# Optimization experiments

Measured on AMD Instinct MI355X. Metric: run time of the kernel, lower is better.

## Reference

```python
import jax, jax.numpy as jnp
import numpy as np

B_, H_, W_, DMODEL = 4, 56, 56, 96
DSTATE = 16
DIN = int(2.0 * DMODEL)      # d_inner = ssm_ratio * d_model
RANK = int(np.ceil(DMODEL / 16))  # dt_rank 'auto'
K = 4                         # 4 scan directions


def setup_inputs() -> dict:
    key = jax.random.key(0)
    ks = jax.random.split(key, 8)
    f = lambda k, shape, s=0.02: jax.random.normal(k, shape, jnp.float32) * s
    x = jax.random.normal(ks[0], (B_, H_, W_, DMODEL), jnp.float32)
    in_proj_w = f(ks[1], (2 * DIN, DMODEL))
    conv_w = f(ks[2], (DIN, 1, 3, 3), 0.1)          # depthwise 3x3
    conv_b = jnp.zeros((DIN,), jnp.float32)
    x_proj_weight = f(ks[3], (K, RANK + 2 * DSTATE, DIN))
    dt_projs_weight = f(ks[4], (K, DIN, RANK), 0.1)
    # dt bias = inverse-softplus of dt sampled log-uniform in [1e-3, 0.1]
    dt = jnp.exp(jax.random.uniform(ks[5], (K, DIN)) * (np.log(0.1) - np.log(0.001)) + np.log(0.001))
    dt_projs_bias = dt + jnp.log(-jnp.expm1(-dt))
    A_logs = jnp.log(jnp.tile(jnp.arange(1, DSTATE + 1, dtype=jnp.float32)[None, :], (K * DIN, 1)))
    Ds = jnp.ones((K * DIN,), jnp.float32)
    ln_gamma = jnp.ones((DIN,), jnp.float32)
    ln_beta = jnp.zeros((DIN,), jnp.float32)
    out_proj_w = f(ks[6], (DMODEL, DIN))
    return dict(x=x, in_proj_w=in_proj_w, conv_w=conv_w, conv_b=conv_b,
                x_proj_weight=x_proj_weight, dt_projs_weight=dt_projs_weight,
                dt_projs_bias=dt_projs_bias, A_logs=A_logs, Ds=Ds,
                ln_gamma=ln_gamma, ln_beta=ln_beta, out_proj_w=out_proj_w)


def _ss2d(x, in_proj_w, conv_w, conv_b, x_proj_weight, dt_projs_weight,
          dt_projs_bias, A_logs, Ds, ln_gamma, ln_beta, out_proj_w):
    B, H, W, _ = x.shape
    L, D, N = H * W, DIN, DSTATE
    # input projection, split into x and gate z
    xz = x @ in_proj_w.T                                   # [B,H,W,2D]
    xc, z = jnp.split(xz, 2, axis=-1)
    z = jax.nn.silu(z)
    # depthwise 3x3 conv (NCHW) + SiLU
    xc = xc.transpose(0, 3, 1, 2)                          # [B,D,H,W]
    xc = jax.lax.conv_general_dilated(
        xc, conv_w, (1, 1), 'SAME',
        dimension_numbers=('NCHW', 'OIHW', 'NCHW'),
        feature_group_count=D) + conv_b[None, :, None, None]
    xc = jax.nn.silu(xc)
    # 4-directional cross scan: HW, WH, and their reverses
    x_hw = xc.reshape(B, D, L)
    x_wh = xc.transpose(0, 1, 3, 2).reshape(B, D, L)
    x2 = jnp.stack([x_hw, x_wh], axis=1)                   # [B,2,D,L]
    xs = jnp.concatenate([x2, jnp.flip(x2, axis=-1)], axis=1)  # [B,K,D,L]
    # per-direction projections to (dt_rank, B, C)
    x_dbl = jnp.einsum('bkdl,kcd->bkcl', xs, x_proj_weight)
    dts, Bs, Cs = jnp.split(x_dbl, [RANK, RANK + N], axis=2)   # [B,K,R|N|N,L]
    dts = jnp.einsum('bkrl,kdr->bkdl', dts, dt_projs_weight)   # [B,K,D,L]
    A = -jnp.exp(A_logs).reshape(K, D, N)
    delta = jax.nn.softplus(dts + dt_projs_bias[None, :, :, None])  # [B,K,D,L]
    # selective state-space scan over L
    u_t = xs.transpose(3, 0, 1, 2)     # [L,B,K,D]
    d_t = delta.transpose(3, 0, 1, 2)  # [L,B,K,D]
    B_t = Bs.transpose(3, 0, 1, 2)     # [L,B,K,N]
    C_t = Cs.transpose(3, 0, 1, 2)     # [L,B,K,N]

    def step(h, inp):
        dt_, u_, b_, c_ = inp
        dA = jnp.exp(dt_[..., None] * A)                       # [B,K,D,N]
        h = dA * h + dt_[..., None] * b_[:, :, None, :] * u_[..., None]
        y = jnp.einsum('bkdn,bkn->bkd', h, c_)
        return h, y

    h0 = jnp.zeros((B, K, D, N), jnp.float32)
    _, ys = jax.lax.scan(step, h0, (d_t, u_t, B_t, C_t))       # ys: [L,B,K,D]
    out_y = ys.transpose(1, 2, 3, 0) + Ds.reshape(K, D)[None, :, :, None] * xs  # [B,K,D,L]
    # merge the 4 directions back into HW order
    inv_y = jnp.flip(out_y[:, 2:4], axis=-1)                   # [B,2,D,L]
    wh_y = out_y[:, 1].reshape(B, D, W, H).transpose(0, 1, 3, 2).reshape(B, D, L)
    invwh_y = inv_y[:, 1].reshape(B, D, W, H).transpose(0, 1, 3, 2).reshape(B, D, L)
    y = out_y[:, 0] + inv_y[:, 0] + wh_y + invwh_y             # [B,D,L]
    y = y.transpose(0, 2, 1)                                   # [B,L,D]
    mu = y.mean(-1, keepdims=True)
    var = y.var(-1, keepdims=True)
    y = (y - mu) * jax.lax.rsqrt(var + 1e-5) * ln_gamma + ln_beta
    y = y.reshape(B, H, W, D) * z
    return y @ out_proj_w.T                                    # [B,H,W,d_model]


def reference(x, in_proj_w, conv_w, conv_b, x_proj_weight, dt_projs_weight,
              dt_projs_bias, A_logs, Ds, ln_gamma, ln_beta, out_proj_w):
    return _ss2d(x, in_proj_w, conv_w, conv_b, x_proj_weight, dt_projs_weight,
                 dt_projs_bias, A_logs, Ds, ln_gamma, ln_beta, out_proj_w)
```

## Files before the change

### kernel.cpp

```cpp
#include <hip/hip_runtime.h>
#include <math.h>

typedef __attribute__((ext_vector_type(2))) float f32x2;
typedef unsigned short u16;

constexpr int BB  = 4;
constexpr int HH  = 56;
constexpr int WW  = 56;
constexpr int CM  = 96;
constexpr int DD  = 192;
constexpr int NS  = 16;
constexpr int KK  = 4;
constexpr int LL  = HH * WW;
constexpr int CH  = 16;
constexpr int NCH = LL / CH;
constexpr int GC  = 7;
constexpr int G   = NCH / GC;
constexpr int PCH = 64;
constexpr int PNCH = LL / PCH;
constexpr int XDS = 40;
constexpr int MR  = 32;
constexpr int YS  = 196;

static __device__ __forceinline__ float siluf(float x) {
  return x / (1.f + __expf(-x));
}
static __device__ __forceinline__ u16 f2bf(float x) {
  unsigned u = __float_as_uint(x);
  u += 0x7fffu + ((u >> 16) & 1u);
  return (u16)(u >> 16);
}
static __device__ __forceinline__ float bf2f(u16 h) {
  return __uint_as_float(((unsigned)h) << 16);
}
static __device__ __forceinline__ unsigned pack2bf(float a, float b) {
  return ((unsigned)f2bf(b) << 16) | f2bf(a);
}
static __device__ __forceinline__ f32x2 up2bf(unsigned v) {
  return (f32x2){__uint_as_float(v << 16),
                 __uint_as_float(v & 0xffff0000u)};
}

__global__ __launch_bounds__(256) void k_prep(
    const float* __restrict__ ipw, const float* __restrict__ xpw,
    float* __restrict__ wTi, float* __restrict__ wtp) {
  int idx = blockIdx.x * 256 + threadIdx.x;
  if (idx < 96 * 384) {
    int k96 = idx / 384, n = idx % 384;
    wTi[idx] = ipw[n * 96 + k96];
  }
  int j = idx - 96 * 384;
  if (j >= 0 && j < KK * DD * 40) {
    int k = j / (DD * 40);
    int r = j % (DD * 40);
    int d = r / 40, ci = r % 40;
    wtp[j] = (ci < 38) ? xpw[((size_t)k * 38 + ci) * DD + d] : 0.f;
  }
}

__global__ __launch_bounds__(256) void k_inproj(
    const float* __restrict__ x, const float* __restrict__ wTi,
    u16* __restrict__ xc16, u16* __restrict__ z16) {
  __shared__ float a[64 * 97];
  const int tid = threadIdx.x;
  const int m0 = blockIdx.x * 64;
  const int y  = blockIdx.y;
  const float4* xv = (const float4*)(x + (size_t)m0 * 96);
#pragma unroll
  for (int i = 0; i < 6; ++i) {
    int idx = tid + i * 256;
    int m = idx / 24, q = idx % 24;
    float4 v = xv[idx];
    a[m * 97 + 4 * q + 0] = v.x; a[m * 97 + 4 * q + 1] = v.y;
    a[m * 97 + 4 * q + 2] = v.z; a[m * 97 + 4 * q + 3] = v.w;
  }
  __syncthreads();
  const int lane = tid & 63;
  const int wid = __builtin_amdgcn_readfirstlane(threadIdx.x >> 6);
  const float* wrow0 = wTi + y * 96 + wid * 24;
  float acc[24];
#pragma unroll
  for (int j = 0; j < 24; ++j) acc[j] = 0.f;
  const float* arow = a + lane * 97;
#pragma unroll 4
  for (int k = 0; k < 96; ++k) {
    float u = arow[k];
    const float* wr = wrow0 + (size_t)k * 384;
#pragma unroll
    for (int j = 0; j < 24; ++j) acc[j] = fmaf(wr[j], u, acc[j]);
  }
  __syncthreads();
#pragma unroll
  for (int j = 0; j < 24; ++j) a[lane * 97 + wid * 24 + j] = acc[j];
  __syncthreads();
  const bool isz = (y >= 2);
  u16* dst = isz ? z16 : xc16;
  const int c0 = (y & 1) * 96;
#pragma unroll
  for (int i = 0; i < 6; ++i) {
    int idx = tid + i * 256;
    int m = idx / 24, q = idx % 24;
    float4 v;
    v.x = a[m * 97 + 4 * q + 0]; v.y = a[m * 97 + 4 * q + 1];
    v.z = a[m * 97 + 4 * q + 2]; v.w = a[m * 97 + 4 * q + 3];
    if (isz) { v.x = siluf(v.x); v.y = siluf(v.y);
               v.z = siluf(v.z); v.w = siluf(v.w); }
    *(uint2*)(dst + (size_t)(m0 + m) * DD + c0 + 4 * q) =
        make_uint2(pack2bf(v.x, v.y), pack2bf(v.z, v.w));
  }
}

__global__ __launch_bounds__(256) void k_conv(
    const u16* __restrict__ xc16, const float* __restrict__ cw,
    const float* __restrict__ cb, u16* __restrict__ xhw16) {
  const int idx = blockIdx.x * 256 + threadIdx.x;
  const int d = idx % DD;
  int t = idx / DD;
  const int w = t % WW;
  t /= WW;
  const int h = t % HH;
  const int b = t / HH;
  const u16* src = xc16 + (size_t)b * LL * DD;
  float acc = cb[d];
#pragma unroll
  for (int dh = -1; dh <= 1; ++dh) {
    int hh = h + dh;
    if (hh < 0 || hh >= HH) continue;
#pragma unroll
    for (int dw = -1; dw <= 1; ++dw) {
      int ww2 = w + dw;
      if (ww2 < 0 || ww2 >= WW) continue;
      acc = fmaf(cw[d * 9 + (dh + 1) * 3 + (dw + 1)],
                 bf2f(src[((size_t)hh * WW + ww2) * DD + d]), acc);
    }
  }
  xhw16[idx] = f2bf(siluf(acc));
}

__global__ __launch_bounds__(256) void k_xdbl(
    const u16* __restrict__ xhw16, const float* __restrict__ wtp,
    u16* __restrict__ xdbl16) {
  const int blk = blockIdx.x;
  const int b = blk / (KK * PNCH);
  const int k = (blk / PNCH) % KK;
  const int c = blk % PNCH;
  const int l0 = c * PCH;
  const bool rev = (k >= 2);
  const int pos = threadIdx.x & 63;
  const int cg = __builtin_amdgcn_readfirstlane(threadIdx.x >> 6);
  int tg = l0 + pos;
  int lg = rev ? (LL - 1 - tg) : tg;
  int row = (k & 1) ? ((lg % HH) * WW + lg / HH) : lg;
  const u16* ur = xhw16 + (size_t)b * LL * DD + (size_t)row * DD;
  const float* wbase = wtp + (size_t)k * DD * 40 + cg * 10;
  float acc[10];
#pragma unroll
  for (int q = 0; q < 10; ++q) acc[q] = 0.f;
#pragma unroll 2
  for (int d8 = 0; d8 < 24; ++d8) {
    uint4 uv = *(const uint4*)(ur + d8 * 8);
    f32x2 u01 = up2bf(uv.x), u23 = up2bf(uv.y);
    f32x2 u45 = up2bf(uv.z), u67 = up2bf(uv.w);
    const float* w0 = wbase + (size_t)(d8 * 8) * 40;
#pragma unroll
    for (int q = 0; q < 10; ++q) acc[q] = fmaf(w0[q],       u01.x, acc[q]);
#pragma unroll
    for (int q = 0; q < 10; ++q) acc[q] = fmaf(w0[40 + q],  u01.y, acc[q]);
#pragma unroll
    for (int q = 0; q < 10; ++q) acc[q] = fmaf(w0[80 + q],  u23.x, acc[q]);
#pragma unroll
    for (int q = 0; q < 10; ++q) acc[q] = fmaf(w0[120 + q], u23.y, acc[q]);
#pragma unroll
    for (int q = 0; q < 10; ++q) acc[q] = fmaf(w0[160 + q], u45.x, acc[q]);
#pragma unroll
    for (int q = 0; q < 10; ++q) acc[q] = fmaf(w0[200 + q], u45.y, acc[q]);
#pragma unroll
    for (int q = 0; q < 10; ++q) acc[q] = fmaf(w0[240 + q], u67.x, acc[q]);
#pragma unroll
    for (int q = 0; q < 10; ++q) acc[q] = fmaf(w0[280 + q], u67.y, acc[q]);
  }
  u16* dst = xdbl16 + ((size_t)(b * KK + k) * LL + l0 + pos) * XDS;
#pragma unroll
  for (int q = 0; q < 10; ++q) {
    int ci = cg * 10 + q;
    int col = ci + (ci >= 6 ? 2 : 0);
    dst[col] = f2bf(acc[q]);
  }
}

static __device__ __forceinline__ int row_init(int k, bool rev, int l0,
                                               int& hh, int& ww) {
  int tg = rev ? (LL - 1 - l0) : l0;
  if (k & 1) {
    hh = tg % HH;
    ww = tg / HH;
    return hh * WW + ww;
  }
  return tg;
}
static __device__ __forceinline__ int row_next(int k, bool rev, int row,
                                               int& hh, int& ww) {
  if (k & 1) {
    if (!rev) { if (++hh == HH) { hh = 0; ++ww; } }
    else      { if (--hh < 0) { hh = HH - 1; --ww; } }
    return hh * WW + ww;
  }
  return rev ? row - 1 : row + 1;
}

__global__ __launch_bounds__(192) void k_scan1(
    const u16* __restrict__ xhw16, const u16* __restrict__ xdbl16,
    const float* __restrict__ dtw, const float* __restrict__ dtb,
    float* __restrict__ Qc, u16* __restrict__ Sc16) {
  __shared__ float us[CH * DD];
  const int blk = blockIdx.x;
  const int b = blk / (KK * NCH);
  const int k = (blk / NCH) % KK;
  const int c = blk % NCH;
  const int l0 = c * CH;
  const bool rev = (k >= 2);
  const int d = threadIdx.x;
  const int bk = b * KK + k;
  {
    const u16* uplane = xhw16 + (size_t)b * LL * DD;
    float tmp[CH];
    int hh, ww;
    int row = row_init(k, rev, l0, hh, ww);
#pragma unroll
    for (int t = 0; t < CH; ++t) {
      tmp[t] = bf2f(uplane[(size_t)row * DD + d]);
      row = row_next(k, rev, row, hh, ww);
    }
#pragma unroll
    for (int t = 0; t < CH; ++t) us[t * DD + d] = tmp[t];
  }
  float w2[6];
#pragma unroll
  for (int r = 0; r < 6; ++r) w2[r] = dtw[((size_t)k * DD + d) * 6 + r];
  const float bias = dtb[k * DD + d];
  f32x2 h2[8];
#pragma unroll
  for (int m = 0; m < 8; ++m) h2[m] = (f32x2){0.f, 0.f};
  float sumd = 0.f;
  const u16* xrow = xdbl16 + ((size_t)bk * LL + l0) * XDS;
  __syncthreads();
#pragma unroll
  for (int t = 0; t < CH; ++t, xrow += XDS) {
    uint4 uv0 = *(const uint4*)(xrow);
    uint4 uv1 = *(const uint4*)(xrow + 8);
    uint4 uv2 = *(const uint4*)(xrow + 16);
    f32x2 d01 = up2bf(uv0.x), d23 = up2bf(uv0.y), d45 = up2bf(uv0.z);
    float u = us[t * DD + d];
    float draw = bias;
    draw = fmaf(w2[0], d01.x, draw);
    draw = fmaf(w2[1], d01.y, draw);
    draw = fmaf(w2[2], d23.x, draw);
    draw = fmaf(w2[3], d23.y, draw);
    draw = fmaf(w2[4], d45.x, draw);
    draw = fmaf(w2[5], d45.y, draw);
    float e = __expf(draw);
    float p = __builtin_amdgcn_rcpf(1.f + e);
    float delta = (draw < 15.f) ? -__logf(p) : draw;
    sumd += delta;
    float du = delta * u;
    f32x2 duv = {du, du};
    float ps = p * p;
    f32x2 pw = {p, ps};
    f32x2 q2 = {ps, ps};
    f32x2 bp[8] = {up2bf(uv1.x), up2bf(uv1.y), up2bf(uv1.z), up2bf(uv1.w),
                   up2bf(uv2.x), up2bf(uv2.y), up2bf(uv2.z), up2bf(uv2.w)};
#pragma unroll
    for (int m = 0; m < 8; ++m) {
      h2[m] = pw * h2[m] + duv * bp[m];
      pw = pw * q2;
    }
  }
  size_t qi = ((size_t)bk * NCH + c) * DD + d;
  Qc[qi] = sumd;
  unsigned* sp = (unsigned*)(Sc16 + qi * 16);
#pragma unroll
  for (int m = 0; m < 8; ++m) sp[m] = pack2bf(h2[m].x, h2[m].y);
}

__global__ __launch_bounds__(256) void k_pfxA(
    const float* __restrict__ Qc, const u16* __restrict__ Sc16,
    u16* __restrict__ Ag16, u16* __restrict__ Sg16) {
  int flat = blockIdx.x * 256 + threadIdx.x;
  int n = flat & 15;
  int d = (flat >> 4) % DD;
  int g = (flat / (NS * DD)) % G;
  int bk = flat / (NS * DD * G);
  const float en = -(float)(n + 1);
  size_t cbase = (size_t)bk * NCH + (size_t)g * GC;
  float q[GC], s[GC];
#pragma unroll
  for (int i = 0; i < GC; ++i) {
    size_t ci = (cbase + i) * DD + d;
    q[i] = Qc[ci];
    s[i] = bf2f(Sc16[ci * 16 + n]);
  }
  float qsum = 0.f, S = 0.f;
#pragma unroll
  for (int i = 0; i < GC; ++i) {
    qsum += q[i];
    S = fmaf(__expf(en * q[i]), S, s[i]);
  }
  Ag16[flat] = f2bf(__expf(en * qsum));
  Sg16[flat] = f2bf(S);
}

__global__ __launch_bounds__(256) void k_pfxB(
    const u16* __restrict__ Ag16, const u16* __restrict__ Sg16,
    u16* __restrict__ Hg16) {
  int flat = blockIdx.x * 256 + threadIdx.x;
  int dn = flat % (DD * NS);
  int bk = flat / (DD * NS);
  const size_t base0 = (size_t)bk * G * DD * NS + dn;
  const size_t gs = DD * NS;
  float av[G], sv[G];
#pragma unroll
  for (int g2 = 0; g2 < G; ++g2) {
    av[g2] = bf2f(Ag16[base0 + (size_t)g2 * gs]);
    sv[g2] = bf2f(Sg16[base0 + (size_t)g2 * gs]);
  }
  float h = 0.f;
#pragma unroll
  for (int g2 = 0; g2 < G; ++g2) {
    Hg16[base0 + (size_t)g2 * gs] = f2bf(h);
    h = fmaf(av[g2], h, sv[g2]);
  }
}

__global__ __launch_bounds__(192) void k_scan2(
    const u16* __restrict__ xhw16, const u16* __restrict__ xdbl16,
    const u16* __restrict__ Hg16, const float* __restrict__ Qc,
    const u16* __restrict__ Sc16, const float* __restrict__ dtw,
    const float* __restrict__ dtb, const float* __restrict__ Ds,
    u16* __restrict__ y16) {
  __shared__ float us[CH * DD];
  const int blk = blockIdx.x;
  const int b = blk / (KK * NCH);
  const int k = (blk / NCH) % KK;
  const int c = blk % NCH;
  const int g = c / GC;
  const int l0 = c * CH;
  const bool rev = (k >= 2);
  const int d = threadIdx.x;
  const int bk = b * KK + k;
  {
    const u16* uplane = xhw16 + (size_t)b * LL * DD;
    float tmp[CH];
    int hh, ww;
    int row = row_init(k, rev, l0, hh, ww);
#pragma unroll
    for (int t = 0; t < CH; ++t) {
      tmp[t] = bf2f(uplane[(size_t)row * DD + d]);
      row = row_next(k, rev, row, hh, ww);
    }
#pragma unroll
    for (int t = 0; t < CH; ++t) us[t * DD + d] = tmp[t];
  }
  float w2[6];
#pragma unroll
  for (int r = 0; r < 6; ++r) w2[r] = dtw[((size_t)k * DD + d) * 6 + r];
  const float bias = dtb[k * DD + d];
  const float dsd = Ds[k * DD + d];
  f32x2 h2[8];
  {
    const u16* hp = Hg16 + (((size_t)bk * G + g) * DD + d) * NS;
    uint4 a0 = *(const uint4*)hp;
    uint4 a1 = *(const uint4*)(hp + 8);
    h2[0] = up2bf(a0.x); h2[1] = up2bf(a0.y);
    h2[2] = up2bf(a0.z); h2[3] = up2bf(a0.w);
    h2[4] = up2bf(a1.x); h2[5] = up2bf(a1.y);
    h2[6] = up2bf(a1.z); h2[7] = up2bf(a1.w);
  }
  for (int i = g * GC; i < c; ++i) {
    size_t ci = ((size_t)bk * NCH + i) * DD + d;
    float r = __expf(-Qc[ci]);
    const u16* sp = Sc16 + ci * 16;
    uint4 s0 = *(const uint4*)sp;
    uint4 s1 = *(const uint4*)(sp + 8);
    f32x2 sv[8] = {up2bf(s0.x), up2bf(s0.y), up2bf(s0.z), up2bf(s0.w),
                   up2bf(s1.x), up2bf(s1.y), up2bf(s1.z), up2bf(s1.w)};
    float r2 = r * r;
    f32x2 pw = {r, r2};
    f32x2 q2 = {r2, r2};
#pragma unroll
    for (int m = 0; m < 8; ++m) {
      h2[m] = pw * h2[m] + sv[m];
      pw = pw * q2;
    }
  }
  u16* yplane = y16 + (size_t)bk * LL * DD + d;
  const u16* xrow = xdbl16 + ((size_t)bk * LL + l0) * XDS;
  int hh, ww;
  int row = row_init(k, rev, l0, hh, ww);
  __syncthreads();
#pragma unroll
  for (int t = 0; t < CH; ++t, xrow += XDS) {
    uint4 uv0 = *(const uint4*)(xrow);
    uint4 uv1 = *(const uint4*)(xrow + 8);
    uint4 uv2 = *(const uint4*)(xrow + 16);
    uint4 uv3 = *(const uint4*)(xrow + 24);
    uint4 uv4 = *(const uint4*)(xrow + 32);
    f32x2 d01 = up2bf(uv0.x), d23 = up2bf(uv0.y), d45 = up2bf(uv0.z);
    float u = us[t * DD + d];
    float draw = bias;
    draw = fmaf(w2[0], d01.x, draw);
    draw = fmaf(w2[1], d01.y, draw);
    draw = fmaf(w2[2], d23.x, draw);
    draw = fmaf(w2[3], d23.y, draw);
    draw = fmaf(w2[4], d45.x, draw);
    draw = fmaf(w2[5], d45.y, draw);
    float e = __expf(draw);
    float p = __builtin_amdgcn_rcpf(1.f + e);
    float delta = (draw < 15.f) ? -__logf(p) : draw;
    float du = delta * u;
    f32x2 duv = {du, du};
    float ps = p * p;
    f32x2 pw = {p, ps};
    f32x2 q2 = {ps, ps};
    f32x2 yacc = {0.f, 0.f};
    f32x2 bp[8] = {up2bf(uv1.x), up2bf(uv1.y), up2bf(uv1.z), up2bf(uv1.w),
                   up2bf(uv2.x), up2bf(uv2.y), up2bf(uv2.z), up2bf(uv2.w)};
    f32x2 cp[8] = {up2bf(uv3.x), up2bf(uv3.y), up2bf(uv3.z), up2bf(uv3.w),
                   up2bf(uv4.x), up2bf(uv4.y), up2bf(uv4.z), up2bf(uv4.w)};
#pragma unroll
    for (int m = 0; m < 8; ++m) {
      h2[m] = pw * h2[m] + duv * bp[m];
      yacc = yacc + h2[m] * cp[m];
      pw = pw * q2;
    }
    yplane[(size_t)row * DD] = f2bf(fmaf(dsd, u, yacc.x + yacc.y));
    row = row_next(k, rev, row, hh, ww);
  }
}

__global__ __launch_bounds__(256) void k_merge_out(
    const u16* __restrict__ y16, const u16* __restrict__ z16,
    const float* __restrict__ gamma, const float* __restrict__ beta,
    const float* __restrict__ wo, float* __restrict__ out) {
  __shared__ float ym[MR][YS];
  __shared__ float ssum[MR][9];
  __shared__ float ssq[MR][9];
  __shared__ float stat[MR][2];
  const int tid = threadIdx.x;
  const int m0 = blockIdx.x * MR;
  const int b = m0 / LL;
  const int lb = m0 % LL;
  const u16* P = y16 + (size_t)b * KK * LL * DD;
  constexpr size_t PL = (size_t)LL * DD;
  for (int idx = tid; idx < MR * (DD / 2); idx += 256) {
    int row = idx / (DD / 2), pr = idx % (DD / 2);
    size_t base = (size_t)(lb + row) * DD + pr * 2;
    float s0 = 0.f, s1 = 0.f;
#pragma unroll
    for (int pl = 0; pl < 4; ++pl) {
      unsigned v = *(const unsigned*)(P + pl * PL + base);
      f32x2 vv = up2bf(v);
      s0 += vv.x; s1 += vv.y;
    }
    *(f32x2*)&ym[row][pr * 2] = (f32x2){s0, s1};
  }
  __syncthreads();
  {
    int r2 = tid & 31, os8 = tid >> 5;
    float s = 0.f, sq = 0.f;
#pragma unroll
    for (int i = 0; i < 24; ++i) {
      float v = ym[r2][os8 * 24 + i];
      s += v; sq = fmaf(v, v, sq);
    }
    ssum[r2][os8] = s; ssq[r2][os8] = sq;
  }
  __syncthreads();
  if (tid < MR) {
    float s = 0.f, sq = 0.f;
#pragma unroll
    for (int i = 0; i < 8; ++i) { s += ssum[tid][i]; sq += ssq[tid][i]; }
    float mean = s * (1.f / DD);
    float var = sq * (1.f / DD) - mean * mean;
    stat[tid][0] = mean;
    stat[tid][1] = rsqrtf(var + 1e-5f);
  }
  __syncthreads();
  for (int idx = tid; idx < MR * DD; idx += 256) {
    int r2 = idx / DD, d = idx % DD;
    float v = (ym[r2][d] - stat[r2][0]) * stat[r2][1] * gamma[d] + beta[d];
    v *= bf2f(z16[(size_t)(m0 + r2) * DD + d]);
    ym[r2][d] = v;
  }
  __syncthreads();
  const int r0 = (tid & 15) * 2;
  const int os = tid >> 4;
  float acc0[6] = {}, acc1[6] = {};
  for (int d4 = 0; d4 < 48; ++d4) {
    float4 a0 = *(const float4*)&ym[r0][d4 * 4];
    float4 a1 = *(const float4*)&ym[r0 + 1][d4 * 4];
#pragma unroll
    for (int j = 0; j < 6; ++j) {
      const float4 w4 =
          *(const float4*)(wo + (size_t)(os * 6 + j) * DD + d4 * 4);
      acc0[j] = fmaf(w4.x, a0.x,
                fmaf(w4.y, a0.y, fmaf(w4.z, a0.z, fmaf(w4.w, a0.w, acc0[j]))));
      acc1[j] = fmaf(w4.x, a1.x,
                fmaf(w4.y, a1.y, fmaf(w4.z, a1.z, fmaf(w4.w, a1.w, acc1[j]))));
    }
  }
  __syncthreads();
#pragma unroll
  for (int j = 0; j < 6; ++j) {
    ym[r0][os * 6 + j] = acc0[j];
    ym[r0 + 1][os * 6 + j] = acc1[j];
  }
  __syncthreads();
  for (int idx = tid; idx < MR * (CM / 4); idx += 256) {
    int r2 = idx / (CM / 4), c4 = idx % (CM / 4);
    float4 v = *(const float4*)&ym[r2][c4 * 4];
    *(float4*)(out + (size_t)(m0 + r2) * CM + c4 * 4) = v;
  }
}

extern "C" void kernel_launch(void* const* d_in, const int* in_sizes, int n_in,
                              void* d_out, int out_size, void* d_ws,
                              size_t ws_size, hipStream_t stream) {
  (void)in_sizes; (void)n_in; (void)out_size; (void)ws_size;
  const float* x   = (const float*)d_in[0];
  const float* ipw = (const float*)d_in[1];
  const float* cw  = (const float*)d_in[2];
  const float* cb  = (const float*)d_in[3];
  const float* xpw = (const float*)d_in[4];
  const float* dtw = (const float*)d_in[5];
  const float* dtb = (const float*)d_in[6];
  const float* Ds  = (const float*)d_in[8];
  const float* gam = (const float*)d_in[9];
  const float* bet = (const float*)d_in[10];
  const float* wo  = (const float*)d_in[11];
  float* out = (float*)d_out;

  char* pb = (char*)d_ws;
  u16* z16   = (u16*)pb; pb += (size_t)BB * LL * DD * 2;
  u16* xc16  = (u16*)pb; pb += (size_t)BB * LL * DD * 2;
  u16* xhw16 = (u16*)pb; pb += (size_t)BB * LL * DD * 2;
  u16* xdbl16 = (u16*)pb; pb += (size_t)BB * KK * LL * XDS * 2;
  float* Qc  = (float*)pb; pb += (size_t)BB * KK * NCH * DD * 4;
  float* wTi = (float*)pb; pb += 96 * 384 * 4;
  float* wtp = (float*)pb; pb += KK * DD * 40 * 4;
  u16* Sc16 = (u16*)pb; pb += (size_t)BB * KK * NCH * DD * NS * 2;
  u16* Ag16 = (u16*)pb; pb += (size_t)BB * KK * G * DD * NS * 2;
  u16* Sg16 = (u16*)pb; pb += (size_t)BB * KK * G * DD * NS * 2;
  u16* Hg16 = (u16*)pb; pb += (size_t)BB * KK * G * DD * NS * 2;
  u16* y16  = (u16*)pb; pb += (size_t)BB * KK * LL * DD * 2;

  k_prep<<<dim3(264), 256, 0, stream>>>(ipw, xpw, wTi, wtp);
  k_inproj<<<dim3(196, 4), 256, 0, stream>>>(x, wTi, xc16, z16);
  k_conv<<<dim3(BB * LL * DD / 256), 256, 0, stream>>>(xc16, cw, cb, xhw16);
  k_xdbl<<<dim3(BB * KK * PNCH), 256, 0, stream>>>(xhw16, wtp, xdbl16);
  k_scan1<<<dim3(BB * KK * NCH), 192, 0, stream>>>(
      xhw16, xdbl16, dtw, dtb, Qc, Sc16);
  k_pfxA<<<dim3(BB * KK * G * DD * NS / 256), 256, 0, stream>>>(
      Qc, Sc16, Ag16, Sg16);
  k_pfxB<<<dim3(BB * KK * DD * NS / 256), 256, 0, stream>>>(
      Ag16, Sg16, Hg16);
  k_scan2<<<dim3(BB * KK * NCH), 192, 0, stream>>>(
      xhw16, xdbl16, Hg16, Qc, Sc16, dtw, dtb, Ds, y16);
  k_merge_out<<<dim3(BB * LL / MR), 256, 0, stream>>>(
      y16, z16, gam, bet, wo, out);
}
```

Before: 242.8 us.

## Compute local chunk outputs in first scan pass, apply carry-in correction in second

The first chunked scan pass now also produces the local (zero-initial-state) output y and the running cumulative delta per step, writing both as bf16 buffers. The second pass no longer recomputes delta, B-projection and the recurrence; it only adds the decayed carry-in state contribution exp(-n*cumdelta)*h0·C to the stored local output. xdbl rows are staged once into shared memory as floats. This removes the duplicated scan arithmetic, but adds two extra full-size bf16 intermediate buffers of global write and read traffic and an extra bf16 rounding of the partial output.

Result: faster. 238.0 us (-2.0%).

```diff
diff --git a/kernel.cpp b/kernel.cpp
--- a/kernel.cpp
+++ b/kernel.cpp
@@ -208,11 +208,14 @@
   return rev ? row - 1 : row + 1;
 }
 
-__global__ __launch_bounds__(192) void k_scan1(
+__global__ __launch_bounds__(192) void k_scanY(
     const u16* __restrict__ xhw16, const u16* __restrict__ xdbl16,
     const float* __restrict__ dtw, const float* __restrict__ dtb,
-    float* __restrict__ Qc, u16* __restrict__ Sc16) {
+    const float* __restrict__ Ds, float* __restrict__ Qc,
+    u16* __restrict__ Sc16, u16* __restrict__ ylc16,
+    u16* __restrict__ cum16) {
   __shared__ float us[CH * DD];
+  __shared__ __align__(16) float xsf[CH * XDS];
   const int blk = blockIdx.x;
   const int b = blk / (KK * NCH);
   const int k = (blk / NCH) % KK;
@@ -222,6 +225,17 @@
   const int d = threadIdx.x;
   const int bk = b * KK + k;
   {
+    const uint4* src = (const uint4*)(xdbl16 + ((size_t)bk * LL + l0) * XDS);
+    if (d < 80) {
+      uint4 uv = src[d];
+      f32x2 p0 = up2bf(uv.x), p1 = up2bf(uv.y);
+      f32x2 p2 = up2bf(uv.z), p3 = up2bf(uv.w);
+      float* w = xsf + d * 8;
+      *(float4*)(w)     = make_float4(p0.x, p0.y, p1.x, p1.y);
+      *(float4*)(w + 4) = make_float4(p2.x, p2.y, p3.x, p3.y);
+    }
+  }
+  {
     const u16* uplane = xhw16 + (size_t)b * LL * DD;
     float tmp[CH];
     int hh, ww;
@@ -238,26 +252,35 @@
 #pragma unroll
   for (int r = 0; r < 6; ++r) w2[r] = dtw[((size_t)k * DD + d) * 6 + r];
   const float bias = dtb[k * DD + d];
+  const float dsd = Ds[k * DD + d];
   f32x2 h2[8];
 #pragma unroll
   for (int m = 0; m < 8; ++m) h2[m] = (f32x2){0.f, 0.f};
   float sumd = 0.f;
-  const u16* xrow = xdbl16 + ((size_t)bk * LL + l0) * XDS;
-  __syncthreads();
-#pragma unroll
-  for (int t = 0; t < CH; ++t, xrow += XDS) {
-    uint4 uv0 = *(const uint4*)(xrow);
-    uint4 uv1 = *(const uint4*)(xrow + 8);
-    uint4 uv2 = *(const uint4*)(xrow + 16);
-    f32x2 d01 = up2bf(uv0.x), d23 = up2bf(uv0.y), d45 = up2bf(uv0.z);
+  u16* ybase = ylc16 + ((size_t)bk * LL + l0) * DD + d;
+  u16* cbase = cum16 + ((size_t)bk * LL + l0) * DD + d;
+  __syncthreads();
+#pragma unroll
+  for (int t = 0; t < CH; ++t) {
+    const float* xr = xsf + t * XDS;
+    float4 fd0 = *(const float4*)(xr);
+    float4 fd1 = *(const float4*)(xr + 4);
+    float4 b0 = *(const float4*)(xr + 8);
+    float4 b1 = *(const float4*)(xr + 12);
+    float4 b2 = *(const float4*)(xr + 16);
+    float4 b3 = *(const float4*)(xr + 20);
+    float4 c0 = *(const float4*)(xr + 24);
+    float4 c1 = *(const float4*)(xr + 28);
+    float4 c2 = *(const float4*)(xr + 32);
+    float4 c3 = *(const float4*)(xr + 36);
     float u = us[t * DD + d];
     float draw = bias;
-    draw = fmaf(w2[0], d01.x, draw);
-    draw = fmaf(w2[1], d01.y, draw);
-    draw = fmaf(w2[2], d23.x, draw);
-    draw = fmaf(w2[3], d23.y, draw);
-    draw = fmaf(w2[4], d45.x, draw);
-    draw = fmaf(w2[5], d45.y, draw);
+    draw = fmaf(w2[0], fd0.x, draw);
+    draw = fmaf(w2[1], fd0.y, draw);
+    draw = fmaf(w2[2], fd0.z, draw);
+    draw = fmaf(w2[3], fd0.w, draw);
+    draw = fmaf(w2[4], fd1.x, draw);
+    draw = fmaf(w2[5], fd1.y, draw);
     float e = __expf(draw);
     float p = __builtin_amdgcn_rcpf(1.f + e);
     float delta = (draw < 15.f) ? -__logf(p) : draw;
@@ -267,13 +290,19 @@
     float ps = p * p;
     f32x2 pw = {p, ps};
     f32x2 q2 = {ps, ps};
-    f32x2 bp[8] = {up2bf(uv1.x), up2bf(uv1.y), up2bf(uv1.z), up2bf(uv1.w),
-                   up2bf(uv2.x), up2bf(uv2.y), up2bf(uv2.z), up2bf(uv2.w)};
+    f32x2 yacc = {0.f, 0.f};
+    f32x2 bp[8] = {{b0.x, b0.y}, {b0.z, b0.w}, {b1.x, b1.y}, {b1.z, b1.w},
+                   {b2.x, b2.y}, {b2.z, b2.w}, {b3.x, b3.y}, {b3.z, b3.w}};
+    f32x2 cp[8] = {{c0.x, c0.y}, {c0.z, c0.w}, {c1.x, c1.y}, {c1.z, c1.w},
+                   {c2.x, c2.y}, {c2.z, c2.w}, {c3.x, c3.y}, {c3.z, c3.w}};
 #pragma unroll
     for (int m = 0; m < 8; ++m) {
       h2[m] = pw * h2[m] + duv * bp[m];
+      yacc = yacc + h2[m] * cp[m];
       pw = pw * q2;
     }
+    ybase[(size_t)t * DD] = f2bf(fmaf(dsd, u, yacc.x + yacc.y));
+    cbase[(size_t)t * DD] = f2bf(sumd);
   }
   size_t qi = ((size_t)bk * NCH + c) * DD + d;
   Qc[qi] = sumd;
@@ -331,13 +360,12 @@
   }
 }
 
-__global__ __launch_bounds__(192) void k_scan2(
-    const u16* __restrict__ xhw16, const u16* __restrict__ xdbl16,
-    const u16* __restrict__ Hg16, const float* __restrict__ Qc,
-    const u16* __restrict__ Sc16, const float* __restrict__ dtw,
-    const float* __restrict__ dtb, const float* __restrict__ Ds,
+__global__ __launch_bounds__(192) void k_correct(
+    const u16* __restrict__ xdbl16, const u16* __restrict__ Hg16,
+    const float* __restrict__ Qc, const u16* __restrict__ Sc16,
+    const u16* __restrict__ ylc16, const u16* __restrict__ cum16,
     u16* __restrict__ y16) {
-  __shared__ float us[CH * DD];
+  __shared__ __align__(16) float cf[CH * 16];
   const int blk = blockIdx.x;
   const int b = blk / (KK * NCH);
   const int k = (blk / NCH) % KK;
@@ -348,23 +376,17 @@
   const int d = threadIdx.x;
   const int bk = b * KK + k;
   {
-    const u16* uplane = xhw16 + (size_t)b * LL * DD;
-    float tmp[CH];
-    int hh, ww;
-    int row = row_init(k, rev, l0, hh, ww);
-#pragma unroll
-    for (int t = 0; t < CH; ++t) {
-      tmp[t] = bf2f(uplane[(size_t)row * DD + d]);
-      row = row_next(k, rev, row, hh, ww);
-    }
-#pragma unroll
-    for (int t = 0; t < CH; ++t) us[t * DD + d] = tmp[t];
-  }
-  float w2[6];
-#pragma unroll
-  for (int r = 0; r < 6; ++r) w2[r] = dtw[((size_t)k * DD + d) * 6 + r];
-  const float bias = dtb[k * DD + d];
-  const float dsd = Ds[k * DD + d];
+    if (d < 32) {
+      int r = d >> 1, half = d & 1;
+      const uint4 uv = *(const uint4*)(
+          xdbl16 + ((size_t)bk * LL + l0 + r) * XDS + 24 + half * 8);
+      f32x2 p0 = up2bf(uv.x), p1 = up2bf(uv.y);
+      f32x2 p2 = up2bf(uv.z), p3 = up2bf(uv.w);
+      float* w = cf + r * 16 + half * 8;
+      *(float4*)(w)     = make_float4(p0.x, p0.y, p1.x, p1.y);
+      *(float4*)(w + 4) = make_float4(p2.x, p2.y, p3.x, p3.y);
+    }
+  }
   f32x2 h2[8];
   {
     const u16* hp = Hg16 + (((size_t)bk * G + g) * DD + d) * NS;
@@ -392,47 +414,29 @@
       pw = pw * q2;
     }
   }
+  const u16* ybase = ylc16 + ((size_t)bk * LL + l0) * DD + d;
+  const u16* cbase = cum16 + ((size_t)bk * LL + l0) * DD + d;
   u16* yplane = y16 + (size_t)bk * LL * DD + d;
-  const u16* xrow = xdbl16 + ((size_t)bk * LL + l0) * XDS;
   int hh, ww;
   int row = row_init(k, rev, l0, hh, ww);
   __syncthreads();
 #pragma unroll
-  for (int t = 0; t < CH; ++t, xrow += XDS) {
-    uint4 uv0 = *(const uint4*)(xrow);
-    uint4 uv1 = *(const uint4*)(xrow + 8);
-    uint4 uv2 = *(const uint4*)(xrow + 16);
-    uint4 uv3 = *(const uint4*)(xrow + 24);
-    uint4 uv4 = *(const uint4*)(xrow + 32);
-    f32x2 d01 = up2bf(uv0.x), d23 = up2bf(uv0.y), d45 = up2bf(uv0.z);
-    float u = us[t * DD + d];
-    float draw = bias;
-    draw = fmaf(w2[0], d01.x, draw);
-    draw = fmaf(w2[1], d01.y, draw);
-    draw = fmaf(w2[2], d23.x, draw);
-    draw = fmaf(w2[3], d23.y, draw);
-    draw = fmaf(w2[4], d45.x, draw);
-    draw = fmaf(w2[5], d45.y, draw);
-    float e = __expf(draw);
-    float p = __builtin_amdgcn_rcpf(1.f + e);
-    float delta = (draw < 15.f) ? -__logf(p) : draw;
-    float du = delta * u;
-    f32x2 duv = {du, du};
-    float ps = p * p;
-    f32x2 pw = {p, ps};
+  for (int t = 0; t < CH; ++t) {
+    float cd = bf2f(cbase[(size_t)t * DD]);
+    float yl = bf2f(ybase[(size_t)t * DD]);
+    float p1 = __expf(-cd);
+    float ps = p1 * p1;
+    f32x2 pw = {p1, ps};
     f32x2 q2 = {ps, ps};
     f32x2 yacc = {0.f, 0.f};
-    f32x2 bp[8] = {up2bf(uv1.x), up2bf(uv1.y), up2bf(uv1.z), up2bf(uv1.w),
-                   up2bf(uv2.x), up2bf(uv2.y), up2bf(uv2.z), up2bf(uv2.w)};
-    f32x2 cp[8] = {up2bf(uv3.x), up2bf(uv3.y), up2bf(uv3.z), up2bf(uv3.w),
-                   up2bf(uv4.x), up2bf(uv4.y), up2bf(uv4.z), up2bf(uv4.w)};
+    const float* cr = cf + t * 16;
 #pragma unroll
     for (int m = 0; m < 8; ++m) {
-      h2[m] = pw * h2[m] + duv * bp[m];
-      yacc = yacc + h2[m] * cp[m];
+      f32x2 cp = *(const f32x2*)(cr + 2 * m);
+      yacc = yacc + (pw * h2[m]) * cp;
       pw = pw * q2;
     }
-    yplane[(size_t)row * DD] = f2bf(fmaf(dsd, u, yacc.x + yacc.y));
+    yplane[(size_t)row * DD] = f2bf(yl + yacc.x + yacc.y);
     row = row_next(k, rev, row, hh, ww);
   }
 }
@@ -551,20 +555,22 @@
   u16* Ag16 = (u16*)pb; pb += (size_t)BB * KK * G * DD * NS * 2;
   u16* Sg16 = (u16*)pb; pb += (size_t)BB * KK * G * DD * NS * 2;
   u16* Hg16 = (u16*)pb; pb += (size_t)BB * KK * G * DD * NS * 2;
+  u16* ylc16 = (u16*)pb; pb += (size_t)BB * KK * LL * DD * 2;
+  u16* cum16 = (u16*)pb; pb += (size_t)BB * KK * LL * DD * 2;
   u16* y16  = (u16*)pb; pb += (size_t)BB * KK * LL * DD * 2;
 
   k_prep<<<dim3(264), 256, 0, stream>>>(ipw, xpw, wTi, wtp);
   k_inproj<<<dim3(196, 4), 256, 0, stream>>>(x, wTi, xc16, z16);
   k_conv<<<dim3(BB * LL * DD / 256), 256, 0, stream>>>(xc16, cw, cb, xhw16);
   k_xdbl<<<dim3(BB * KK * PNCH), 256, 0, stream>>>(xhw16, wtp, xdbl16);
-  k_scan1<<<dim3(BB * KK * NCH), 192, 0, stream>>>(
-      xhw16, xdbl16, dtw, dtb, Qc, Sc16);
+  k_scanY<<<dim3(BB * KK * NCH), 192, 0, stream>>>(
+      xhw16, xdbl16, dtw, dtb, Ds, Qc, Sc16, ylc16, cum16);
   k_pfxA<<<dim3(BB * KK * G * DD * NS / 256), 256, 0, stream>>>(
       Qc, Sc16, Ag16, Sg16);
   k_pfxB<<<dim3(BB * KK * DD * NS / 256), 256, 0, stream>>>(
       Ag16, Sg16, Hg16);
-  k_scan2<<<dim3(BB * KK * NCH), 192, 0, stream>>>(
-      xhw16, xdbl16, Hg16, Qc, Sc16, dtw, dtb, Ds, y16);
+  k_correct<<<dim3(BB * KK * NCH), 192, 0, stream>>>(
+      xdbl16, Hg16, Qc, Sc16, ylc16, cum16, y16);
   k_merge_out<<<dim3(BB * LL / MR), 256, 0, stream>>>(
       y16, z16, gam, bet, wo, out);
 }
```
